# Kernel tuning notes

Measured on AMD Instinct MI355X. Metric: run time of the kernel, lower is better.

The kernel has to match this reference:

```python
import math
import jax, jax.numpy as jnp
import numpy as np

B, N, D, PE = 4, 512, 32, 16
K_SHARP = 10.0  # module arg k: sigmoid sharpness for energy-difference sign


def setup_inputs() -> dict:
    key = jax.random.key(0)
    ks = jax.random.split(key, 8)
    # h is a density-like positive field (log is taken in forward)
    h = jax.random.uniform(ks[0], (B, N, D), jnp.float32, 1e-3, 1.0)
    pe = jax.random.normal(ks[1], (B, N, PE), jnp.float32)
    E = jax.random.normal(ks[2], (N,), jnp.float32)  # node energies
    A = jax.random.bernoulli(ks[3], 0.1, (N, N)).astype(jnp.float32)  # adjacency mask
    s = 1.0 / math.sqrt(PE)
    Wk = jax.random.normal(ks[4], (PE, D), jnp.float32) * s  # w_k.weight^T
    bk = jnp.zeros((D,), jnp.float32)
    Wq = jax.random.normal(ks[5], (PE, D), jnp.float32) * s  # w_q.weight^T
    bq = jnp.zeros((D,), jnp.float32)
    beta = jax.random.uniform(ks[6], (D,), jnp.float32)  # nn.Parameter(torch.rand(nhidden))
    return {"t": 0, "h": h, "pe": pe, "E": E, "A": A,
            "Wk": Wk, "bk": bk, "Wq": Wq, "bq": bq, "beta": beta}


def reference(t, h, pe, E, A, Wk, bk, Wq, bq, beta):
    """Fokker-Planck on graph ODE function in log space. t is unused (autonomous)."""
    _, _, d = h.shape
    log_h = jnp.log(h + 1e-8)                              # [B,N,D]
    K = pe @ Wk + bk                                       # [B,N,D]
    Q = pe @ Wq + bq                                       # [B,N,D]
    scores = A[None] * jnp.einsum('bid,bjd->bij', K, Q) / math.sqrt(d)
    W = jax.nn.softmax(scores, axis=-1)                    # [B,N,N], softmax over j
    E_diff = E[None, :] - E[:, None]                       # [i,j] = E[j] - E[i]
    # [b,i,j,d] = log_h[b,j,d] - log_h[b,i,d]
    log_h_diff = log_h[:, None, :, :] - log_h[:, :, None, :]
    drift = W[..., None] * (E_diff[None, :, :, None] + beta * log_h_diff)
    sign = jax.nn.sigmoid(K_SHARP * E_diff)                # [N,N]
    sgn = sign[None, :, :, None]
    # upwind-style blend: sign*h[b,j,:] + (1-sign)*h[b,i,:]
    weighted_h = sgn * h[:, None, :, :] + (1.0 - sgn) * h[:, :, None, :]
    dh_dt = jnp.sum(drift * weighted_h, axis=2)            # sum over j -> [B,N,D]
    return dh_dt
```

## Files before the change

kernel.cpp:

```cpp
#include <hip/hip_runtime.h>
#include <math.h>

constexpr int NB = 4;
constexpr int NN = 512;
constexpr int ND = 32;
constexpr int NPE = 16;
constexpr float INV_SQRT_D = 0.17677669529663687f;
constexpr float KSHARP = 10.0f;
constexpr float LN2 = 0.69314718055994531f;

__global__ __launch_bounds__(512, 4) void fpg_kernel(
    const float* __restrict__ h,
    const float* __restrict__ pe,
    const float* __restrict__ E,
    const float* __restrict__ A,
    const float* __restrict__ Wk,
    const float* __restrict__ bk,
    const float* __restrict__ Wq,
    const float* __restrict__ bq,
    const float* __restrict__ beta,
    float* __restrict__ out)
{
    const int blk = blockIdx.x;
    const int b   = blk >> 7;
    const int i0  = (blk & 127) << 2;
    const int t   = threadIdx.x;

    __shared__ __align__(16) float sK[4][ND];
    __shared__ float sKWq[4][20];
    __shared__ __align__(16) float sCoef[NN][3][4];
    __shared__ float sPart[4][2][4];
    __shared__ float sS1[4], sS3[4];
    __shared__ float sRed[16][4][ND];

    const float* h_b  = h  + (size_t)b * NN * ND;
    const float* pe_b = pe + (size_t)b * NN * NPE;

    if (t < 128) {
        const int r = t >> 5, d = t & 31;
        const float* pe_i = pe_b + (size_t)(i0 + r) * NPE;
        float k = bk[d];
        #pragma unroll
        for (int p = 0; p < NPE; ++p) k = fmaf(pe_i[p], Wk[p * ND + d], k);
        sK[r][d] = k;
    }
    __syncthreads();

    if (t < 128) {
        const int r = t >> 5, q = t & 31;
        if (q < 17) {
            const float* wrow = (q < 16) ? (Wq + q * ND) : bq;
            float acc = 0.f;
            #pragma unroll
            for (int d = 0; d < ND; ++d) acc = fmaf(sK[r][d], wrow[d], acc);
            sKWq[r][q] = acc;
        }
    }
    __syncthreads();

    const int r    = t >> 7;
    const int jj   = t & 127;
    const int i    = i0 + r;
    const int lane = t & 63;
    const int wh   = (t >> 6) & 1;

    float kq[17];
    #pragma unroll
    for (int p = 0; p < 17; ++p) kq[p] = sKWq[r][p];
    const float Ei = E[i];
    const float* Arow = A + (size_t)i * NN;

    float sc[4], ed[4], sg[4];
    #pragma unroll
    for (int k = 0; k < 4; ++k) {
        const int j = jj + (k << 7);
        const float4* pj = (const float4*)(pe_b + (size_t)j * NPE);
        const float4 p0 = pj[0], p1 = pj[1], p2 = pj[2], p3 = pj[3];
        float dot = kq[16];
        dot = fmaf(p0.x, kq[0],  dot); dot = fmaf(p0.y, kq[1],  dot);
        dot = fmaf(p0.z, kq[2],  dot); dot = fmaf(p0.w, kq[3],  dot);
        dot = fmaf(p1.x, kq[4],  dot); dot = fmaf(p1.y, kq[5],  dot);
        dot = fmaf(p1.z, kq[6],  dot); dot = fmaf(p1.w, kq[7],  dot);
        dot = fmaf(p2.x, kq[8],  dot); dot = fmaf(p2.y, kq[9],  dot);
        dot = fmaf(p2.z, kq[10], dot); dot = fmaf(p2.w, kq[11], dot);
        dot = fmaf(p3.x, kq[12], dot); dot = fmaf(p3.y, kq[13], dot);
        dot = fmaf(p3.z, kq[14], dot); dot = fmaf(p3.w, kq[15], dot);
        sc[k] = Arow[j] * dot * INV_SQRT_D;
        const float e = E[j] - Ei;
        ed[k] = e;
        sg[k] = 1.0f / (1.0f + __expf(-KSHARP * e));
    }

    float m = fmaxf(fmaxf(sc[0], sc[1]), fmaxf(sc[2], sc[3]));
    #pragma unroll
    for (int off = 32; off >= 1; off >>= 1) m = fmaxf(m, __shfl_xor(m, off));
    if (lane == 0) sPart[r][wh][0] = m;
    __syncthreads();
    const float M = fmaxf(sPart[r][0][0], sPart[r][1][0]);

    float eh[4];
    float s0 = 0.f, s1 = 0.f, s2 = 0.f;
    #pragma unroll
    for (int k = 0; k < 4; ++k) {
        eh[k] = __expf(sc[k] - M);
        const float om = 1.0f - sg[k];
        s0 += eh[k];
        s1 += eh[k] * ed[k] * om;
        s2 += eh[k] * om;
    }
    #pragma unroll
    for (int off = 32; off >= 1; off >>= 1) {
        s0 += __shfl_xor(s0, off);
        s1 += __shfl_xor(s1, off);
        s2 += __shfl_xor(s2, off);
    }
    if (lane == 0) { sPart[r][wh][1] = s0; sPart[r][wh][2] = s1; sPart[r][wh][3] = s2; }
    __syncthreads();
    const float S   = sPart[r][0][1] + sPart[r][1][1];
    const float inv = 1.0f / S;
    if ((t & 127) == 0) {
        sS1[r] = (sPart[r][0][2] + sPart[r][1][2]) * inv;
        sS3[r] = (sPart[r][0][3] + sPart[r][1][3]) * inv;
    }

    #pragma unroll
    for (int k = 0; k < 4; ++k) {
        const int j = jj + (k << 7);
        const float w  = eh[k] * inv;
        const float c4 = w * sg[k];
        const float c3 = w - c4;
        const float c2 = w * ed[k] * sg[k];
        sCoef[j][0][r] = c2;
        sCoef[j][1][r] = c3;
        sCoef[j][2][r] = c4;
    }
    __syncthreads();

    const int d = t & 31, g = t >> 5;
    const float b2 = beta[d] * LN2;
    float vA2[4] = {0,0,0,0}, vA3[4] = {0,0,0,0};
    float vA4[4] = {0,0,0,0}, vA5[4] = {0,0,0,0};
    #pragma unroll 4
    for (int q = 0; q < 32; ++q) {
        const int j = (q << 4) + g;
        const float4 C2 = *(const float4*)sCoef[j][0];
        const float4 C3 = *(const float4*)sCoef[j][1];
        const float4 C4 = *(const float4*)sCoef[j][2];
        const float hv = h_b[(size_t)j * ND + d];
        const float L2 = __log2f(hv + 1e-8f);
        const float hL = hv * L2;
        vA2[0] = fmaf(C2.x, hv, vA2[0]); vA2[1] = fmaf(C2.y, hv, vA2[1]);
        vA2[2] = fmaf(C2.z, hv, vA2[2]); vA2[3] = fmaf(C2.w, hv, vA2[3]);
        vA3[0] = fmaf(C3.x, L2, vA3[0]); vA3[1] = fmaf(C3.y, L2, vA3[1]);
        vA3[2] = fmaf(C3.z, L2, vA3[2]); vA3[3] = fmaf(C3.w, L2, vA3[3]);
        vA4[0] = fmaf(C4.x, hL, vA4[0]); vA4[1] = fmaf(C4.y, hL, vA4[1]);
        vA4[2] = fmaf(C4.z, hL, vA4[2]); vA4[3] = fmaf(C4.w, hL, vA4[3]);
        vA5[0] = fmaf(C4.x, hv, vA5[0]); vA5[1] = fmaf(C4.y, hv, vA5[1]);
        vA5[2] = fmaf(C4.z, hv, vA5[2]); vA5[3] = fmaf(C4.w, hv, vA5[3]);
    }
    #pragma unroll
    for (int rr = 0; rr < 4; ++rr) {
        const float hi  = h_b[(size_t)(i0 + rr) * ND + d];
        const float L2i = __log2f(hi + 1e-8f);
        const float p = vA2[rr] + b2 * (vA4[rr] + hi * vA3[rr] - L2i * vA5[rr]);
        sRed[g][rr][d] = p;
    }
    __syncthreads();

    if (t < 128) {
        const int rr = t >> 5, dd = t & 31;
        float sum = 0.f;
        #pragma unroll
        for (int g2 = 0; g2 < 16; ++g2) sum += sRed[g2][rr][dd];
        const float hi  = h_b[(size_t)(i0 + rr) * ND + dd];
        const float L2i = __log2f(hi + 1e-8f);
        const float b2d = beta[dd] * LN2;
        out[(size_t)(b * NN + i0 + rr) * ND + dd] =
            sum + hi * (sS1[rr] - b2d * L2i * sS3[rr]);
    }
}

extern "C" void kernel_launch(void* const* d_in, const int* in_sizes, int n_in,
                              void* d_out, int out_size, void* d_ws, size_t ws_size,
                              hipStream_t stream) {
    const float* h    = (const float*)d_in[1];
    const float* pe   = (const float*)d_in[2];
    const float* E    = (const float*)d_in[3];
    const float* A    = (const float*)d_in[4];
    const float* Wk   = (const float*)d_in[5];
    const float* bk   = (const float*)d_in[6];
    const float* Wq   = (const float*)d_in[7];
    const float* bq   = (const float*)d_in[8];
    const float* beta = (const float*)d_in[9];
    float* out = (float*)d_out;

    fpg_kernel<<<NB * NN / 4, 512, 0, stream>>>(pe ? h : h, pe, E, A, Wk, bk, Wq, bq, beta, out);
}
```

Baseline: 17.02 us.

## Remap accumulation loop to 2 rows × 4 dims per thread with float4 h loads

Restructures the main j-accumulation so each thread handles two target rows and four contiguous hidden dims, loading h as float4 and row-pair coefficients as float2. The shared coefficient layout and the padded reduction buffer change to match, and the final reduction now sums over 32 groups. This aims to cut per-j LDS traffic and scalar global loads. In exchange, each thread recomputes log2 for every h element it reads, which doubles the log evaluations across the block and raises register use.

```diff
diff --git a/kernel.cpp b/kernel.cpp
--- a/kernel.cpp
+++ b/kernel.cpp
@@ -28,10 +28,10 @@
 
     __shared__ __align__(16) float sK[4][ND];
     __shared__ float sKWq[4][20];
-    __shared__ __align__(16) float sCoef[NN][3][4];
+    __shared__ __align__(16) float sCoefP[3][2][NN][2];
     __shared__ float sPart[4][2][4];
     __shared__ float sS1[4], sS3[4];
-    __shared__ float sRed[16][4][ND];
+    __shared__ __align__(16) float4 sRed4[32][33];
 
     const float* h_b  = h  + (size_t)b * NN * ND;
     const float* pe_b = pe + (size_t)b * NN * NPE;
@@ -123,6 +123,7 @@
         sS3[r] = (sPart[r][0][3] + sPart[r][1][3]) * inv;
     }
 
+    const int rp = r >> 1, ri = r & 1;
     #pragma unroll
     for (int k = 0; k < 4; ++k) {
         const int j = jj + (k << 7);
@@ -130,48 +131,67 @@
         const float c4 = w * sg[k];
         const float c3 = w - c4;
         const float c2 = w * ed[k] * sg[k];
-        sCoef[j][0][r] = c2;
-        sCoef[j][1][r] = c3;
-        sCoef[j][2][r] = c4;
-    }
-    __syncthreads();
-
-    const int d = t & 31, g = t >> 5;
-    const float b2 = beta[d] * LN2;
-    float vA2[4] = {0,0,0,0}, vA3[4] = {0,0,0,0};
-    float vA4[4] = {0,0,0,0}, vA5[4] = {0,0,0,0};
-    #pragma unroll 4
-    for (int q = 0; q < 32; ++q) {
-        const int j = (q << 4) + g;
-        const float4 C2 = *(const float4*)sCoef[j][0];
-        const float4 C3 = *(const float4*)sCoef[j][1];
-        const float4 C4 = *(const float4*)sCoef[j][2];
-        const float hv = h_b[(size_t)j * ND + d];
-        const float L2 = __log2f(hv + 1e-8f);
-        const float hL = hv * L2;
-        vA2[0] = fmaf(C2.x, hv, vA2[0]); vA2[1] = fmaf(C2.y, hv, vA2[1]);
-        vA2[2] = fmaf(C2.z, hv, vA2[2]); vA2[3] = fmaf(C2.w, hv, vA2[3]);
-        vA3[0] = fmaf(C3.x, L2, vA3[0]); vA3[1] = fmaf(C3.y, L2, vA3[1]);
-        vA3[2] = fmaf(C3.z, L2, vA3[2]); vA3[3] = fmaf(C3.w, L2, vA3[3]);
-        vA4[0] = fmaf(C4.x, hL, vA4[0]); vA4[1] = fmaf(C4.y, hL, vA4[1]);
-        vA4[2] = fmaf(C4.z, hL, vA4[2]); vA4[3] = fmaf(C4.w, hL, vA4[3]);
-        vA5[0] = fmaf(C4.x, hv, vA5[0]); vA5[1] = fmaf(C4.y, hv, vA5[1]);
-        vA5[2] = fmaf(C4.z, hv, vA5[2]); vA5[3] = fmaf(C4.w, hv, vA5[3]);
-    }
-    #pragma unroll
-    for (int rr = 0; rr < 4; ++rr) {
-        const float hi  = h_b[(size_t)(i0 + rr) * ND + d];
-        const float L2i = __log2f(hi + 1e-8f);
-        const float p = vA2[rr] + b2 * (vA4[rr] + hi * vA3[rr] - L2i * vA5[rr]);
-        sRed[g][rr][d] = p;
+        sCoefP[0][rp][j][ri] = c2;
+        sCoefP[1][rp][j][ri] = c3;
+        sCoefP[2][rp][j][ri] = c4;
+    }
+    __syncthreads();
+
+    const int rh = t >> 8;
+    const int dq = t & 7;
+    const int d0 = dq << 2;
+    const int g  = (t >> 3) & 31;
+
+    float acc[2][4][4] = {};
+    #pragma unroll
+    for (int q = 0; q < 16; ++q) {
+        const int j = (q << 5) + g;
+        const float2 C2 = *(const float2*)&sCoefP[0][rh][j][0];
+        const float2 C3 = *(const float2*)&sCoefP[1][rh][j][0];
+        const float2 C4 = *(const float2*)&sCoefP[2][rh][j][0];
+        const float4 hv4 = *(const float4*)(h_b + (size_t)j * ND + d0);
+        const float hvv[4] = {hv4.x, hv4.y, hv4.z, hv4.w};
+        const float cc2[2] = {C2.x, C2.y};
+        const float cc3[2] = {C3.x, C3.y};
+        const float cc4[2] = {C4.x, C4.y};
+        #pragma unroll
+        for (int c = 0; c < 4; ++c) {
+            const float hvc = hvv[c];
+            const float l2  = __log2f(hvc + 1e-8f);
+            const float hl  = hvc * l2;
+            #pragma unroll
+            for (int r2 = 0; r2 < 2; ++r2) {
+                acc[r2][0][c] = fmaf(cc2[r2], hvc, acc[r2][0][c]);
+                acc[r2][1][c] = fmaf(cc3[r2], l2,  acc[r2][1][c]);
+                acc[r2][2][c] = fmaf(cc4[r2], hl,  acc[r2][2][c]);
+                acc[r2][3][c] = fmaf(cc4[r2], hvc, acc[r2][3][c]);
+            }
+        }
+    }
+    const float4 bet = *(const float4*)(beta + d0);
+    const float b2v[4] = {bet.x * LN2, bet.y * LN2, bet.z * LN2, bet.w * LN2};
+    #pragma unroll
+    for (int r2 = 0; r2 < 2; ++r2) {
+        const int row = (rh << 1) + r2;
+        const float4 hi4 = *(const float4*)(h_b + (size_t)(i0 + row) * ND + d0);
+        const float hiv[4] = {hi4.x, hi4.y, hi4.z, hi4.w};
+        float pv[4];
+        #pragma unroll
+        for (int c = 0; c < 4; ++c) {
+            const float L2i = __log2f(hiv[c] + 1e-8f);
+            pv[c] = acc[r2][0][c] + b2v[c] * (acc[r2][2][c] + hiv[c] * acc[r2][1][c]
+                                              - L2i * acc[r2][3][c]);
+        }
+        sRed4[g][row * 8 + dq] = make_float4(pv[0], pv[1], pv[2], pv[3]);
     }
     __syncthreads();
 
     if (t < 128) {
         const int rr = t >> 5, dd = t & 31;
+        const float* pR = (const float*)sRed4;
         float sum = 0.f;
         #pragma unroll
-        for (int g2 = 0; g2 < 16; ++g2) sum += sRed[g2][rr][dd];
+        for (int g2 = 0; g2 < 32; ++g2) sum += pR[g2 * 132 + rr * 32 + dd];
         const float hi  = h_b[(size_t)(i0 + rr) * ND + dd];
         const float L2i = __log2f(hi + 1e-8f);
         const float b2d = beta[dd] * LN2;
@@ -194,5 +214,5 @@
     const float* beta = (const float*)d_in[9];
     float* out = (float*)d_out;
 
-    fpg_kernel<<<NB * NN / 4, 512, 0, stream>>>(pe ? h : h, pe, E, A, Wk, bk, Wq, bq, beta, out);
+    fpg_kernel<<<NB * NN / 4, 512, 0, stream>>>(h, pe, E, A, Wk, bk, Wq, bq, beta, out);
 }
```

After: 17.01 us (median of 2 runs). Within noise of the previous version (-0.1%).
